# Kernel tuning notes

Hardware: AMD Instinct MI355X
Metric: run time of the kernel (lower is better)

Reference implementation:

```python
import jax, jax.numpy as jnp
import numpy as np

B, SQ, SK = 2, 2048, 2048
D = 1024            # in_features == num_heads * head_size
H, HS = 16, 64      # num_heads, head_size
SCALE = HS ** -0.5


def setup_inputs() -> dict:
    key = jax.random.key(0)
    ks = jax.random.split(key, 10)
    s = 0.02
    return {
        "inputs": jax.random.normal(ks[0], (B, SQ, D), jnp.float32),
        "context": jax.random.normal(ks[1], (B, SK, D), jnp.float32),
        "Wq": jax.random.normal(ks[2], (D, D), jnp.float32) * s,
        "bq": jnp.zeros((D,), jnp.float32),
        "Wk": jax.random.normal(ks[3], (D, D), jnp.float32) * s,
        "bk": jnp.zeros((D,), jnp.float32),
        "Wv": jax.random.normal(ks[4], (D, D), jnp.float32) * s,
        "bv": jnp.zeros((D,), jnp.float32),
        "Wo": jax.random.normal(ks[5], (D, D), jnp.float32) * s,
        "bo": jnp.zeros((D,), jnp.float32),
    }


def reference(inputs, context, Wq, bq, Wk, bk, Wv, bv, Wo, bo):
    # QKV projections (torch Linear: x @ W.T + b; here W stored as [in, out])
    q = inputs @ Wq + bq            # [B, SQ, D]
    k = context @ Wk + bk           # [B, SK, D]
    v = context @ Wv + bv           # [B, SK, D]
    q = q.reshape(B, SQ, H, HS)
    k = k.reshape(B, SK, H, HS)
    v = v.reshape(B, SK, H, HS)
    # scores: [B, H, SQ, SK] -- full score matrix materialized (as in source)
    score = jnp.einsum("bqhd,bkhd->bhqk", q, k) * SCALE
    weights = jax.nn.softmax(score, axis=-1)
    attn = jnp.einsum("bhqk,bkhd->bqhd", weights, v)  # [B, SQ, H, HS]
    out = attn.reshape(B, SQ, H * HS)
    return out @ Wo + bo
```

## Files before the change

kernel.cpp:

```cpp
#include <hip/hip_runtime.h>

#define BB 2
#define SQ 2048
#define SK 2048
#define DD 1024
#define HH 16
#define HS 64
#define SCALE 0.125f
#define LOG2E 1.4426950408889634f

typedef __bf16 bf16x8 __attribute__((ext_vector_type(8)));
typedef float f32x4 __attribute__((ext_vector_type(4)));
typedef unsigned int uint;

#if defined(__has_builtin)
#if __has_builtin(__builtin_amdgcn_exp2f)
#define FEXP2(x) __builtin_amdgcn_exp2f(x)
#endif
#endif
#ifndef FEXP2
extern "C" __device__ float __ocml_native_exp2_f32(float);
#define FEXP2(x) __ocml_native_exp2_f32(x)
#endif

__device__ __forceinline__ void gload_lds16(const __bf16* g, __bf16* l) {
    __builtin_amdgcn_global_load_lds((const __attribute__((address_space(1))) uint*)(g),
                                     (__attribute__((address_space(3))) uint*)(l), 16, 0, 0);
}

__global__ void wtrans(const float* __restrict__ W0, const float* __restrict__ W1,
                       const float* __restrict__ W2, const float* __restrict__ W3,
                       __bf16* __restrict__ Wt) {
    __shared__ __bf16 tile[32][33];
    const float* W = blockIdx.z == 0 ? W0 : blockIdx.z == 1 ? W1 : blockIdx.z == 2 ? W2 : W3;
    __bf16* out = Wt + (size_t)blockIdx.z * DD * DD;
    int tx = threadIdx.x, ty = threadIdx.y;
    int k0 = blockIdx.y * 32, n0 = blockIdx.x * 32;
#pragma unroll
    for (int j = 0; j < 4; ++j)
        tile[ty + j * 8][tx] = (__bf16)W[(size_t)(k0 + ty + j * 8) * DD + n0 + tx];
    __syncthreads();
#pragma unroll
    for (int j = 0; j < 4; ++j) {
        int n = n0 + ty + j * 8;
        int k = k0 + tx;
        int kswz = (k & ~63) | ((((k >> 3) ^ n) & 7) << 3) | (k & 7);
        out[(size_t)n * DD + kswz] = tile[tx][ty + j * 8];
    }
}

__global__ __launch_bounds__(256, 4) void gemm_qkv(
        const float* __restrict__ Ain, const float* __restrict__ Actx,
        const __bf16* __restrict__ Wt,
        const float* __restrict__ bq, const float* __restrict__ bk, const float* __restrict__ bv,
        __bf16* __restrict__ Qb, __bf16* __restrict__ Kb, __bf16* __restrict__ Vtb,
        float qscale) {
    __shared__ __bf16 As[64][64];
    __shared__ __bf16 Bs[128][64];
    int t = threadIdx.x, w = t >> 6, l = t & 63;
    int lm = l & 15, lk = l >> 4;
    int wr = w >> 1, wc = w & 1;
    int flat = blockIdx.x + 16 * blockIdx.y;
    int nf = (flat & 7) * 192 + (flat >> 3);
    bool isQ = nf < 512;
    int bc, br;
    if (isQ) { bc = nf & 7; br = nf >> 3; }
    else     { int f = nf - 512; bc = f & 15; br = f >> 4; }

    int ra = t >> 2, ca = (t & 3) * 2;
    const float* ag = (isQ ? Ain : Actx) + (size_t)(br * 64 + ra) * 1024 + ca * 8;
    __bf16* aw0 = &As[ra][((ca)     ^ (ra & 7)) * 8];
    __bf16* aw1 = &As[ra][((ca + 1) ^ (ra & 7)) * 8];

    int rb = t >> 3, c8 = t & 7;
    const __bf16 *bg0, *bg1, *bg2, *bg3;
    if (isQ) {
        const __bf16* Wq_ = Wt;
        bg0 = Wq_ + (size_t)(bc * 128 + rb)      * 1024 + c8 * 8;
        bg1 = Wq_ + (size_t)(bc * 128 + rb + 32) * 1024 + c8 * 8;
        bg2 = Wq_ + (size_t)(bc * 128 + rb + 64) * 1024 + c8 * 8;
        bg3 = Wq_ + (size_t)(bc * 128 + rb + 96) * 1024 + c8 * 8;
    } else {
        const __bf16* Wk_ = Wt + (size_t)DD * DD;
        const __bf16* Wv_ = Wt + (size_t)2 * DD * DD;
        bg0 = Wk_ + (size_t)(bc * 64 + rb)      * 1024 + c8 * 8;
        bg1 = Wk_ + (size_t)(bc * 64 + rb + 32) * 1024 + c8 * 8;
        bg2 = Wv_ + (size_t)(bc * 64 + rb)      * 1024 + c8 * 8;
        bg3 = Wv_ + (size_t)(bc * 64 + rb + 32) * 1024 + c8 * 8;
    }
    __bf16* bw0 = &Bs[rb][c8 * 8];
    __bf16* bw1 = &Bs[rb + 32][c8 * 8];
    __bf16* bw2 = &Bs[rb + 64][c8 * 8];
    __bf16* bw3 = &Bs[rb + 96][c8 * 8];

    int brow[4];
#pragma unroll
    for (int n = 0; n < 4; ++n)
        brow[n] = isQ ? (wc * 64 + n * 16 + lm)
                      : ((n >> 1) * 64 + wc * 32 + (n & 1) * 16 + lm);

    float4 xa0, xa1, xa2, xa3, xb0, xb1, xb2, xb3;
#define G_LOAD()                                                                      \
    xa0 = *(const float4*)(ag);     xa1 = *(const float4*)(ag + 4);                   \
    xa2 = *(const float4*)(ag + 8); xa3 = *(const float4*)(ag + 12);                  \
    xb0 = *(const float4*)bg0; xb1 = *(const float4*)bg1;                             \
    xb2 = *(const float4*)bg2; xb3 = *(const float4*)bg3;                             \
    ag += 64; bg0 += 64; bg1 += 64; bg2 += 64; bg3 += 64;
#define G_WRITE()                                                                     \
    {                                                                                 \
        bf16x8 va0 = {(__bf16)xa0.x, (__bf16)xa0.y, (__bf16)xa0.z, (__bf16)xa0.w,     \
                      (__bf16)xa1.x, (__bf16)xa1.y, (__bf16)xa1.z, (__bf16)xa1.w};    \
        bf16x8 va1 = {(__bf16)xa2.x, (__bf16)xa2.y, (__bf16)xa2.z, (__bf16)xa2.w,     \
                      (__bf16)xa3.x, (__bf16)xa3.y, (__bf16)xa3.z, (__bf16)xa3.w};    \
        *(bf16x8*)aw0 = va0; *(bf16x8*)aw1 = va1;                                     \
        *(float4*)bw0 = xb0; *(float4*)bw1 = xb1;                                     \
        *(float4*)bw2 = xb2; *(float4*)bw3 = xb3;                                     \
    }

    f32x4 acc[2][4] = {};
    G_LOAD();
    for (int kt = 0; kt < 1024; kt += 64) {
        __syncthreads();
        G_WRITE();
        __syncthreads();
        if (kt + 64 < 1024) { G_LOAD(); }
#pragma unroll
        for (int kk = 0; kk < 64; kk += 32) {
            int ch = ((kk >> 3) + lk);
            bf16x8 af[2], bf[4];
#pragma unroll
            for (int m = 0; m < 2; ++m)
                af[m] = *(const bf16x8*)&As[wr * 32 + m * 16 + lm][(ch ^ (lm & 7)) * 8];
#pragma unroll
            for (int n = 0; n < 4; ++n)
                bf[n] = *(const bf16x8*)&Bs[brow[n]][(ch ^ (lm & 7)) * 8];
#pragma unroll
            for (int m = 0; m < 2; ++m)
#pragma unroll
                for (int n = 0; n < 4; ++n)
                    acc[m][n] = __builtin_amdgcn_mfma_f32_16x16x32_bf16(af[m], bf[n], acc[m][n], 0, 0, 0);
        }
    }
#undef G_LOAD
#undef G_WRITE

    if (isQ) {
#pragma unroll
        for (int m = 0; m < 2; ++m)
#pragma unroll
            for (int n = 0; n < 4; ++n) {
                int col = bc * 128 + wc * 64 + n * 16 + lm;
                float bb = bq[col];
#pragma unroll
                for (int r = 0; r < 4; ++r) {
                    int row = br * 64 + wr * 32 + m * 16 + lk * 4 + r;
                    Qb[(size_t)row * 1024 + col] = (__bf16)((acc[m][n][r] + bb) * qscale);
                }
            }
    } else {
#pragma unroll
        for (int m = 0; m < 2; ++m)
#pragma unroll
            for (int n = 0; n < 4; ++n) {
                int col = bc * 64 + wc * 32 + (n & 1) * 16 + lm;
                if (n < 2) {
                    float bb = bk[col];
#pragma unroll
                    for (int r = 0; r < 4; ++r) {
                        int row = br * 64 + wr * 32 + m * 16 + lk * 4 + r;
                        Kb[(size_t)row * 1024 + col] = (__bf16)(acc[m][n][r] + bb);
                    }
                } else {
                    float bb = bv[col];
                    int row = br * 64 + wr * 32 + m * 16 + lk * 4;
                    int b_ = row >> 11, sk = row & 2047;
                    int skb = sk & ~63, o = sk & 63;
                    int p0 = (o & 32) | (((o >> 3) & 1) << 4) | (((o >> 2) & 1) << 3) | (((o >> 4) & 1) << 2);
                    int h_ = col >> 6, d_ = col & 63;
                    union { ushort4 u; __bf16 hh[4]; } pk;
#pragma unroll
                    for (int r = 0; r < 4; ++r) pk.hh[r] = (__bf16)(acc[m][n][r] + bb);
                    *(ushort4*)(Vtb + ((size_t)((b_ * 16 + h_) * 64 + d_) * 2048 + skb + p0)) = pk.u;
                }
            }
    }
}

__global__ __launch_bounds__(256) void gemm_out64(const __bf16* __restrict__ A, const __bf16* __restrict__ Bt,
                                                  const float* __restrict__ bias, float* __restrict__ C) {
    __shared__ __bf16 As[64][64];
    __shared__ __bf16 Bs[128][64];
    int t = threadIdx.x;
    int w = t >> 6, l = t & 63;
    int lm = l & 15, lk = l >> 4;
    int flat = blockIdx.x + 8 * blockIdx.y;
    int nf = (flat & 7) * 64 + (flat >> 3);
    int bc = nf & 7, br = nf >> 3;
    int srow = (l >> 3), scol = (l & 7) * 8;
    f32x4 acc[4][2] = {};
    for (int kt = 0; kt < 1024; kt += 64) {
        __syncthreads();
#pragma unroll
        for (int j = 0; j < 2; ++j) {
            int r0 = (j * 4 + w) * 8;
            gload_lds16(&A[(size_t)(br * 64 + r0 + srow) * 1024 + kt + scol], &As[r0][0]);
        }
#pragma unroll
        for (int j = 0; j < 4; ++j) {
            int r0 = (j * 4 + w) * 8;
            gload_lds16(&Bt[(size_t)(bc * 128 + r0 + srow) * 1024 + kt + scol], &Bs[r0][0]);
        }
        __syncthreads();
#pragma unroll
        for (int kk = 0; kk < 64; kk += 32) {
            int ch = ((kk >> 3) + lk);
            bf16x8 af[4], bf[2];
#pragma unroll
            for (int m = 0; m < 4; ++m) af[m] = *(const bf16x8*)&As[m * 16 + lm][kk + lk * 8];
#pragma unroll
            for (int n = 0; n < 2; ++n)
                bf[n] = *(const bf16x8*)&Bs[w * 32 + n * 16 + lm][(ch ^ (lm & 7)) * 8];
#pragma unroll
            for (int m = 0; m < 4; ++m)
#pragma unroll
                for (int n = 0; n < 2; ++n)
                    acc[m][n] = __builtin_amdgcn_mfma_f32_16x16x32_bf16(af[m], bf[n], acc[m][n], 0, 0, 0);
        }
    }
#pragma unroll
    for (int m = 0; m < 4; ++m)
#pragma unroll
        for (int n = 0; n < 2; ++n) {
            int col = bc * 128 + w * 32 + n * 16 + lm;
            float bv = bias[col];
#pragma unroll
            for (int r = 0; r < 4; ++r) {
                int row = br * 64 + m * 16 + lk * 4 + r;
                C[(size_t)row * 1024 + col] = acc[m][n][r] + bv;
            }
        }
}

__global__ __launch_bounds__(512) void flash_attn(const __bf16* __restrict__ Q,
                                                  const __bf16* __restrict__ Kb,
                                                  const __bf16* __restrict__ Vt,
                                                  __bf16* __restrict__ O) {
    __shared__ __bf16 Ks[2][64 * 64];
    __shared__ __bf16 Vs[2][64 * 64];
    int t = threadIdx.x, w = t >> 6, l = t & 63;
    int lm = l & 15, lk = l >> 4;
    int flat = blockIdx.x + 16 * blockIdx.y;
    int nf = (flat & 7) * 64 + (flat >> 3);
    int bh = nf >> 4, b = bh >> 4, h = bh & 15;
    int q0 = (nf & 15) * 128;

    bf16x8 qf[2];
#pragma unroll
    for (int kk = 0; kk < 2; ++kk)
        qf[kk] = *(const bf16x8*)&Q[(size_t)(b * SQ + q0 + w * 16 + lm) * DD + h * HS + kk * 32 + lk * 8];

    int r0 = t >> 3, c8 = t & 7;
    int chs = c8 ^ (r0 & 7);
    __bf16* ksl0 = &Ks[0][r0 * 64 + chs * 8];
    __bf16* vsl0 = &Vs[0][r0 * 64 + chs * 8];

    const __bf16* kp0 = Kb + (size_t)b * SK * DD + h * HS + (size_t)r0 * DD + c8 * 8;
    const __bf16* vp0 = Vt + (size_t)bh * HS * SK + (size_t)r0 * SK + c8 * 8;

    int o0 = lm * 64 + ((lk ^ (lm & 7)) * 8);
    int o1 = lm * 64 + (((4 + lk) ^ (lm & 7)) * 8);

    float4 kr0, vr0;
#define FA_LOAD()                                                                \
    kr0 = *(const float4*)kp0; vr0 = *(const float4*)vp0;                        \
    kp0 += (size_t)64 * DD; vp0 += 64;
#define FA_WRITE(BUF)                                                            \
    *(float4*)(ksl0 + (BUF) * 4096) = kr0;                                       \
    *(float4*)(vsl0 + (BUF) * 4096) = vr0;

    FA_LOAD();
    FA_WRITE(0);
    __syncthreads();

    bf16x8 ones;
#pragma unroll
    for (int j = 0; j < 8; ++j) ones[j] = (__bf16)1.0f;

    f32x4 o[4] = {};
    f32x4 o_s = {};

    for (int it = 0; it < 32; ++it) {
        int buf = it & 1;
        if (it + 1 < 32) { FA_LOAD(); }

        const __bf16* KsB = &Ks[buf][0];
        const __bf16* VsB = &Vs[buf][0];

        f32x4 st[4] = {};
        __builtin_amdgcn_s_setprio(1);
#pragma unroll
        for (int kk = 0; kk < 2; ++kk) {
#pragma unroll
            for (int n = 0; n < 4; ++n) {
                bf16x8 kf = *(const bf16x8*)&KsB[(kk ? o1 : o0) + n * 1024];
                st[n] = __builtin_amdgcn_mfma_f32_16x16x32_bf16(kf, qf[kk], st[n], 0, 0, 0);
            }
        }
        __builtin_amdgcn_s_setprio(0);

#pragma unroll
        for (int kk = 0; kk < 2; ++kk) {
            bf16x8 pa;
#pragma unroll
            for (int j = 0; j < 8; ++j)
                pa[j] = (__bf16)FEXP2(st[2 * kk + (j >> 2)][j & 3]);
            __builtin_amdgcn_s_setprio(1);
            o_s = __builtin_amdgcn_mfma_f32_16x16x32_bf16(pa, ones, o_s, 0, 0, 0);
#pragma unroll
            for (int dn = 0; dn < 4; ++dn) {
                bf16x8 vf = *(const bf16x8*)&VsB[(kk ? o1 : o0) + dn * 1024];
                o[dn] = __builtin_amdgcn_mfma_f32_16x16x32_bf16(pa, vf, o[dn], 0, 0, 0);
            }
            __builtin_amdgcn_s_setprio(0);
        }

        if (it + 1 < 32) { FA_WRITE(buf ^ 1); }
        __syncthreads();
    }

    f32x4 inv;
#pragma unroll
    for (int r = 0; r < 4; ++r) inv[r] = 1.f / o_s[r];
#pragma unroll
    for (int dn = 0; dn < 4; ++dn)
#pragma unroll
        for (int r = 0; r < 4; ++r) {
            int row = q0 + w * 16 + lk * 4 + r;
            int col = h * HS + dn * 16 + lm;
            O[(size_t)(b * SQ + row) * DD + col] = (__bf16)(o[dn][r] * inv[r]);
        }
}

extern "C" void kernel_launch(void* const* d_in, const int* in_sizes, int n_in,
                              void* d_out, int out_size, void* d_ws, size_t ws_size,
                              hipStream_t stream) {
    const float* inputs  = (const float*)d_in[0];
    const float* context = (const float*)d_in[1];
    const float* Wq = (const float*)d_in[2];
    const float* bq = (const float*)d_in[3];
    const float* Wk = (const float*)d_in[4];
    const float* bk = (const float*)d_in[5];
    const float* Wv = (const float*)d_in[6];
    const float* bv = (const float*)d_in[7];
    const float* Wo = (const float*)d_in[8];
    const float* bo = (const float*)d_in[9];
    float* out = (float*)d_out;

    char* ws = (char*)d_ws;
    const size_t SEG = (size_t)4096 * 1024 * sizeof(__bf16);
    __bf16* attb = (__bf16*)(ws + 0 * SEG);
    __bf16* Wt   = (__bf16*)(ws + 2 * SEG);
    __bf16* Qb   = (__bf16*)(ws + 3 * SEG);
    __bf16* Kbuf = (__bf16*)(ws + 4 * SEG);
    __bf16* Vtb  = (__bf16*)(ws + 5 * SEG);

    wtrans<<<dim3(32, 32, 4), dim3(32, 8), 0, stream>>>(Wq, Wk, Wv, Wo, Wt);

    gemm_qkv<<<dim3(16, 96), 256, 0, stream>>>(inputs, context, Wt, bq, bk, bv,
                                               Qb, Kbuf, Vtb, SCALE * LOG2E);

    flash_attn<<<dim3(16, 32), 512, 0, stream>>>(Qb, Kbuf, Vtb, attb);

    gemm_out64<<<dim3(8, 64), 256, 0, stream>>>(attb, Wt + (size_t)3 * DD * DD, bo, out);
}
```

Before: 113.8 us.

## Double-buffer shared memory in QKV projection GEMM to drop one barrier

Double-buffers the A and B shared-memory tiles in the QKV projection GEMM. The next tile's global loads are issued before the MFMA loop and written into the alternate buffer afterward, so each iteration needs one barrier instead of two. This doubles LDS use (48KB per block) and lowers the launch-bounds occupancy hint from 4 to 3 blocks, which may cut latency hiding.

```diff
diff --git a/kernel.cpp b/kernel.cpp
--- a/kernel.cpp
+++ b/kernel.cpp
@@ -49,14 +49,14 @@
     }
 }
 
-__global__ __launch_bounds__(256, 4) void gemm_qkv(
+__global__ __launch_bounds__(256, 3) void gemm_qkv(
         const float* __restrict__ Ain, const float* __restrict__ Actx,
         const __bf16* __restrict__ Wt,
         const float* __restrict__ bq, const float* __restrict__ bk, const float* __restrict__ bv,
         __bf16* __restrict__ Qb, __bf16* __restrict__ Kb, __bf16* __restrict__ Vtb,
         float qscale) {
-    __shared__ __bf16 As[64][64];
-    __shared__ __bf16 Bs[128][64];
+    __shared__ __bf16 As[2 * 64 * 64];
+    __shared__ __bf16 Bs[2 * 128 * 64];
     int t = threadIdx.x, w = t >> 6, l = t & 63;
     int lm = l & 15, lk = l >> 4;
     int wr = w >> 1, wc = w & 1;
@@ -69,8 +69,8 @@
 
     int ra = t >> 2, ca = (t & 3) * 2;
     const float* ag = (isQ ? Ain : Actx) + (size_t)(br * 64 + ra) * 1024 + ca * 8;
-    __bf16* aw0 = &As[ra][((ca)     ^ (ra & 7)) * 8];
-    __bf16* aw1 = &As[ra][((ca + 1) ^ (ra & 7)) * 8];
+    __bf16* aw0 = &As[ra * 64 + ((ca)     ^ (ra & 7)) * 8];
+    __bf16* aw1 = &As[ra * 64 + ((ca + 1) ^ (ra & 7)) * 8];
 
     int rb = t >> 3, c8 = t & 7;
     const __bf16 *bg0, *bg1, *bg2, *bg3;
@@ -88,10 +88,10 @@
         bg2 = Wv_ + (size_t)(bc * 64 + rb)      * 1024 + c8 * 8;
         bg3 = Wv_ + (size_t)(bc * 64 + rb + 32) * 1024 + c8 * 8;
     }
-    __bf16* bw0 = &Bs[rb][c8 * 8];
-    __bf16* bw1 = &Bs[rb + 32][c8 * 8];
-    __bf16* bw2 = &Bs[rb + 64][c8 * 8];
-    __bf16* bw3 = &Bs[rb + 96][c8 * 8];
+    __bf16* bw0 = &Bs[(rb)      * 64 + c8 * 8];
+    __bf16* bw1 = &Bs[(rb + 32) * 64 + c8 * 8];
+    __bf16* bw2 = &Bs[(rb + 64) * 64 + c8 * 8];
+    __bf16* bw3 = &Bs[(rb + 96) * 64 + c8 * 8];
 
     int brow[4];
 #pragma unroll
@@ -106,40 +106,46 @@
     xb0 = *(const float4*)bg0; xb1 = *(const float4*)bg1;                             \
     xb2 = *(const float4*)bg2; xb3 = *(const float4*)bg3;                             \
     ag += 64; bg0 += 64; bg1 += 64; bg2 += 64; bg3 += 64;
-#define G_WRITE()                                                                     \
+#define G_WRITE(BUF)                                                                  \
     {                                                                                 \
         bf16x8 va0 = {(__bf16)xa0.x, (__bf16)xa0.y, (__bf16)xa0.z, (__bf16)xa0.w,     \
                       (__bf16)xa1.x, (__bf16)xa1.y, (__bf16)xa1.z, (__bf16)xa1.w};    \
         bf16x8 va1 = {(__bf16)xa2.x, (__bf16)xa2.y, (__bf16)xa2.z, (__bf16)xa2.w,     \
                       (__bf16)xa3.x, (__bf16)xa3.y, (__bf16)xa3.z, (__bf16)xa3.w};    \
-        *(bf16x8*)aw0 = va0; *(bf16x8*)aw1 = va1;                                     \
-        *(float4*)bw0 = xb0; *(float4*)bw1 = xb1;                                     \
-        *(float4*)bw2 = xb2; *(float4*)bw3 = xb3;                                     \
+        *(bf16x8*)(aw0 + (BUF) * 4096) = va0;                                         \
+        *(bf16x8*)(aw1 + (BUF) * 4096) = va1;                                         \
+        *(float4*)(bw0 + (BUF) * 8192) = xb0;                                         \
+        *(float4*)(bw1 + (BUF) * 8192) = xb1;                                         \
+        *(float4*)(bw2 + (BUF) * 8192) = xb2;                                         \
+        *(float4*)(bw3 + (BUF) * 8192) = xb3;                                         \
     }
 
     f32x4 acc[2][4] = {};
     G_LOAD();
+    G_WRITE(0);
+    __syncthreads();
     for (int kt = 0; kt < 1024; kt += 64) {
-        __syncthreads();
-        G_WRITE();
-        __syncthreads();
-        if (kt + 64 < 1024) { G_LOAD(); }
+        int buf = (kt >> 6) & 1;
+        bool more = (kt + 64 < 1024);
+        if (more) { G_LOAD(); }
 #pragma unroll
         for (int kk = 0; kk < 64; kk += 32) {
             int ch = ((kk >> 3) + lk);
             bf16x8 af[2], bf[4];
 #pragma unroll
             for (int m = 0; m < 2; ++m)
-                af[m] = *(const bf16x8*)&As[wr * 32 + m * 16 + lm][(ch ^ (lm & 7)) * 8];
+                af[m] = *(const bf16x8*)&As[buf * 4096 + (wr * 32 + m * 16 + lm) * 64 + (ch ^ (lm & 7)) * 8];
 #pragma unroll
             for (int n = 0; n < 4; ++n)
-                bf[n] = *(const bf16x8*)&Bs[brow[n]][(ch ^ (lm & 7)) * 8];
+                bf[n] = *(const bf16x8*)&Bs[buf * 8192 + brow[n] * 64 + (ch ^ (lm & 7)) * 8];
 #pragma unroll
             for (int m = 0; m < 2; ++m)
 #pragma unroll
                 for (int n = 0; n < 4; ++n)
                     acc[m][n] = __builtin_amdgcn_mfma_f32_16x16x32_bf16(af[m], bf[n], acc[m][n], 0, 0, 0);
         }
+        if (more) { G_WRITE(buf ^ 1); }
+        __syncthreads();
     }
 #undef G_LOAD
 #undef G_WRITE
```

Measured after the change: 117.4 us. 1.03x slower.

## Double-buffer QKV and output GEMMs with direct global-to-LDS loads

Applied to the files above, without the earlier changes.

Both projection GEMMs now use two LDS buffers, issuing global_load_lds for the next K tile while MFMAs run on the current one, with one barrier per iteration instead of two. The QKV GEMM stages raw fp32 activations into LDS with an XOR swizzle and converts to bf16 at fragment-read time, dropping the register round trip. The output GEMM gains an A-side swizzle that the bf16 tile previously lacked. The cost is twice the LDS per block (the QKV A buffer grows further because it holds fp32), which can reduce occupancy; the QKV kernel also drops its min-blocks launch bound.

```diff
diff --git a/kernel.cpp b/kernel.cpp
--- a/kernel.cpp
+++ b/kernel.cpp
@@ -27,6 +27,10 @@
     __builtin_amdgcn_global_load_lds((const __attribute__((address_space(1))) uint*)(g),
                                      (__attribute__((address_space(3))) uint*)(l), 16, 0, 0);
 }
+__device__ __forceinline__ void gload_lds16f(const float* g, float* l) {
+    __builtin_amdgcn_global_load_lds((const __attribute__((address_space(1))) uint*)(g),
+                                     (__attribute__((address_space(3))) uint*)(l), 16, 0, 0);
+}
 
 __global__ void wtrans(const float* __restrict__ W0, const float* __restrict__ W1,
                        const float* __restrict__ W2, const float* __restrict__ W3,
@@ -49,14 +53,14 @@
     }
 }
 
-__global__ __launch_bounds__(256, 4) void gemm_qkv(
+__global__ __launch_bounds__(256) void gemm_qkv(
         const float* __restrict__ Ain, const float* __restrict__ Actx,
         const __bf16* __restrict__ Wt,
         const float* __restrict__ bq, const float* __restrict__ bk, const float* __restrict__ bv,
         __bf16* __restrict__ Qb, __bf16* __restrict__ Kb, __bf16* __restrict__ Vtb,
         float qscale) {
-    __shared__ __bf16 As[64][64];
-    __shared__ __bf16 Bs[128][64];
+    __shared__ float  Asf[2 * 64 * 64];
+    __shared__ __bf16 Bs[2 * 128 * 64];
     int t = threadIdx.x, w = t >> 6, l = t & 63;
     int lm = l & 15, lk = l >> 4;
     int wr = w >> 1, wc = w & 1;
@@ -67,31 +71,29 @@
     if (isQ) { bc = nf & 7; br = nf >> 3; }
     else     { int f = nf - 512; bc = f & 15; br = f >> 4; }
 
-    int ra = t >> 2, ca = (t & 3) * 2;
-    const float* ag = (isQ ? Ain : Actx) + (size_t)(br * 64 + ra) * 1024 + ca * 8;
-    __bf16* aw0 = &As[ra][((ca)     ^ (ra & 7)) * 8];
-    __bf16* aw1 = &As[ra][((ca + 1) ^ (ra & 7)) * 8];
-
-    int rb = t >> 3, c8 = t & 7;
-    const __bf16 *bg0, *bg1, *bg2, *bg3;
+    int rA = t >> 4, cA = t & 15;
+    int csA = cA ^ (2 * (rA & 7));
+    const float* Afp = isQ ? Ain : Actx;
+    const float* agb = Afp + (size_t)(br * 64 + rA) * 1024 + csA * 4;
+    float* adst = &Asf[rA * 64 + cA * 4];
+
+    int rB = t >> 3, cB = t & 7;
+    const __bf16 *bs0, *bs1, *bs2, *bs3;
     if (isQ) {
         const __bf16* Wq_ = Wt;
-        bg0 = Wq_ + (size_t)(bc * 128 + rb)      * 1024 + c8 * 8;
-        bg1 = Wq_ + (size_t)(bc * 128 + rb + 32) * 1024 + c8 * 8;
-        bg2 = Wq_ + (size_t)(bc * 128 + rb + 64) * 1024 + c8 * 8;
-        bg3 = Wq_ + (size_t)(bc * 128 + rb + 96) * 1024 + c8 * 8;
+        bs0 = Wq_ + (size_t)(bc * 128 + rB)      * 1024 + cB * 8;
+        bs1 = Wq_ + (size_t)(bc * 128 + rB + 32) * 1024 + cB * 8;
+        bs2 = Wq_ + (size_t)(bc * 128 + rB + 64) * 1024 + cB * 8;
+        bs3 = Wq_ + (size_t)(bc * 128 + rB + 96) * 1024 + cB * 8;
     } else {
         const __bf16* Wk_ = Wt + (size_t)DD * DD;
         const __bf16* Wv_ = Wt + (size_t)2 * DD * DD;
-        bg0 = Wk_ + (size_t)(bc * 64 + rb)      * 1024 + c8 * 8;
-        bg1 = Wk_ + (size_t)(bc * 64 + rb + 32) * 1024 + c8 * 8;
-        bg2 = Wv_ + (size_t)(bc * 64 + rb)      * 1024 + c8 * 8;
-        bg3 = Wv_ + (size_t)(bc * 64 + rb + 32) * 1024 + c8 * 8;
-    }
-    __bf16* bw0 = &Bs[rb][c8 * 8];
-    __bf16* bw1 = &Bs[rb + 32][c8 * 8];
-    __bf16* bw2 = &Bs[rb + 64][c8 * 8];
-    __bf16* bw3 = &Bs[rb + 96][c8 * 8];
+        bs0 = Wk_ + (size_t)(bc * 64 + rB)      * 1024 + cB * 8;
+        bs1 = Wk_ + (size_t)(bc * 64 + rB + 32) * 1024 + cB * 8;
+        bs2 = Wv_ + (size_t)(bc * 64 + rB)      * 1024 + cB * 8;
+        bs3 = Wv_ + (size_t)(bc * 64 + rB + 32) * 1024 + cB * 8;
+    }
+    __bf16* bdst = &Bs[rB * 64 + cB * 8];
 
     int brow[4];
 #pragma unroll
@@ -99,50 +101,48 @@
         brow[n] = isQ ? (wc * 64 + n * 16 + lm)
                       : ((n >> 1) * 64 + wc * 32 + (n & 1) * 16 + lm);
 
-    float4 xa0, xa1, xa2, xa3, xb0, xb1, xb2, xb3;
-#define G_LOAD()                                                                      \
-    xa0 = *(const float4*)(ag);     xa1 = *(const float4*)(ag + 4);                   \
-    xa2 = *(const float4*)(ag + 8); xa3 = *(const float4*)(ag + 12);                  \
-    xb0 = *(const float4*)bg0; xb1 = *(const float4*)bg1;                             \
-    xb2 = *(const float4*)bg2; xb3 = *(const float4*)bg3;                             \
-    ag += 64; bg0 += 64; bg1 += 64; bg2 += 64; bg3 += 64;
-#define G_WRITE()                                                                     \
-    {                                                                                 \
-        bf16x8 va0 = {(__bf16)xa0.x, (__bf16)xa0.y, (__bf16)xa0.z, (__bf16)xa0.w,     \
-                      (__bf16)xa1.x, (__bf16)xa1.y, (__bf16)xa1.z, (__bf16)xa1.w};    \
-        bf16x8 va1 = {(__bf16)xa2.x, (__bf16)xa2.y, (__bf16)xa2.z, (__bf16)xa2.w,     \
-                      (__bf16)xa3.x, (__bf16)xa3.y, (__bf16)xa3.z, (__bf16)xa3.w};    \
-        *(bf16x8*)aw0 = va0; *(bf16x8*)aw1 = va1;                                     \
-        *(float4*)bw0 = xb0; *(float4*)bw1 = xb1;                                     \
-        *(float4*)bw2 = xb2; *(float4*)bw3 = xb3;                                     \
-    }
+#define STAGE(BUF, KT)                                                                \
+    gload_lds16f(agb + (KT),             adst + (BUF) * 4096);                        \
+    gload_lds16f(agb + 16384 + (KT),     adst + (BUF) * 4096 + 1024);                 \
+    gload_lds16f(agb + 32768 + (KT),     adst + (BUF) * 4096 + 2048);                 \
+    gload_lds16f(agb + 49152 + (KT),     adst + (BUF) * 4096 + 3072);                 \
+    gload_lds16(bs0 + (KT), bdst + (BUF) * 8192);                                     \
+    gload_lds16(bs1 + (KT), bdst + (BUF) * 8192 + 2048);                              \
+    gload_lds16(bs2 + (KT), bdst + (BUF) * 8192 + 4096);                              \
+    gload_lds16(bs3 + (KT), bdst + (BUF) * 8192 + 6144);
 
     f32x4 acc[2][4] = {};
-    G_LOAD();
-    for (int kt = 0; kt < 1024; kt += 64) {
-        __syncthreads();
-        G_WRITE();
-        __syncthreads();
-        if (kt + 64 < 1024) { G_LOAD(); }
-#pragma unroll
-        for (int kk = 0; kk < 64; kk += 32) {
-            int ch = ((kk >> 3) + lk);
+    STAGE(0, 0);
+    __syncthreads();
+    for (int ts = 0; ts < 16; ++ts) {
+        int buf = ts & 1;
+        if (ts + 1 < 16) { STAGE(buf ^ 1, (ts + 1) * 64); }
+#pragma unroll
+        for (int kk = 0; kk < 2; ++kk) {
             bf16x8 af[2], bf[4];
 #pragma unroll
-            for (int m = 0; m < 2; ++m)
-                af[m] = *(const bf16x8*)&As[wr * 32 + m * 16 + lm][(ch ^ (lm & 7)) * 8];
+            for (int m = 0; m < 2; ++m) {
+                int rr = wr * 32 + m * 16 + lm;
+                int c0 = (kk * 8 + 2 * lk) ^ (2 * (lm & 7));
+                const float* ap = &Asf[buf * 4096 + rr * 64 + c0 * 4];
+                f32x4 lo = *(const f32x4*)ap;
+                f32x4 hi = *(const f32x4*)(ap + 4);
+                af[m] = bf16x8{(__bf16)lo[0], (__bf16)lo[1], (__bf16)lo[2], (__bf16)lo[3],
+                               (__bf16)hi[0], (__bf16)hi[1], (__bf16)hi[2], (__bf16)hi[3]};
+            }
+            int ch = kk * 4 + lk;
 #pragma unroll
             for (int n = 0; n < 4; ++n)
-                bf[n] = *(const bf16x8*)&Bs[brow[n]][(ch ^ (lm & 7)) * 8];
+                bf[n] = *(const bf16x8*)&Bs[buf * 8192 + brow[n] * 64 + ((ch ^ (lm & 7)) * 8)];
 #pragma unroll
             for (int m = 0; m < 2; ++m)
 #pragma unroll
                 for (int n = 0; n < 4; ++n)
                     acc[m][n] = __builtin_amdgcn_mfma_f32_16x16x32_bf16(af[m], bf[n], acc[m][n], 0, 0, 0);
         }
-    }
-#undef G_LOAD
-#undef G_WRITE
+        __syncthreads();
+    }
+#undef STAGE
 
     if (isQ) {
 #pragma unroll
@@ -188,45 +188,55 @@
 
 __global__ __launch_bounds__(256) void gemm_out64(const __bf16* __restrict__ A, const __bf16* __restrict__ Bt,
                                                   const float* __restrict__ bias, float* __restrict__ C) {
-    __shared__ __bf16 As[64][64];
-    __shared__ __bf16 Bs[128][64];
+    __shared__ __bf16 As[2 * 64 * 64];
+    __shared__ __bf16 Bs[2 * 128 * 64];
     int t = threadIdx.x;
     int w = t >> 6, l = t & 63;
     int lm = l & 15, lk = l >> 4;
     int flat = blockIdx.x + 8 * blockIdx.y;
     int nf = (flat & 7) * 64 + (flat >> 3);
     int bc = nf & 7, br = nf >> 3;
-    int srow = (l >> 3), scol = (l & 7) * 8;
+
+    int rA = t >> 3, cA = t & 7;
+    int csA = cA ^ (rA & 7);
+    const __bf16* as0 = A + (size_t)(br * 64 + rA) * 1024 + csA * 8;
+    __bf16* adst = &As[rA * 64 + cA * 8];
+    const __bf16* bs0 = Bt + (size_t)(bc * 128 + rA) * 1024 + cA * 8;
+    __bf16* bdst = &Bs[rA * 64 + cA * 8];
+
+#define STAGE(BUF, KT)                                                                \
+    gload_lds16(as0 + (KT),             adst + (BUF) * 4096);                         \
+    gload_lds16(as0 + 32768 + (KT),     adst + (BUF) * 4096 + 2048);                  \
+    gload_lds16(bs0 + (KT),             bdst + (BUF) * 8192);                         \
+    gload_lds16(bs0 + 32768 + (KT),     bdst + (BUF) * 8192 + 2048);                  \
+    gload_lds16(bs0 + 65536 + (KT),     bdst + (BUF) * 8192 + 4096);                  \
+    gload_lds16(bs0 + 98304 + (KT),     bdst + (BUF) * 8192 + 6144);
+
     f32x4 acc[4][2] = {};
-    for (int kt = 0; kt < 1024; kt += 64) {
-        __syncthreads();
-#pragma unroll
-        for (int j = 0; j < 2; ++j) {
-            int r0 = (j * 4 + w) * 8;
-            gload_lds16(&A[(size_t)(br * 64 + r0 + srow) * 1024 + kt + scol], &As[r0][0]);
-        }
-#pragma unroll
-        for (int j = 0; j < 4; ++j) {
-            int r0 = (j * 4 + w) * 8;
-            gload_lds16(&Bt[(size_t)(bc * 128 + r0 + srow) * 1024 + kt + scol], &Bs[r0][0]);
-        }
-        __syncthreads();
-#pragma unroll
-        for (int kk = 0; kk < 64; kk += 32) {
-            int ch = ((kk >> 3) + lk);
+    STAGE(0, 0);
+    __syncthreads();
+    for (int ts = 0; ts < 16; ++ts) {
+        int buf = ts & 1;
+        if (ts + 1 < 16) { STAGE(buf ^ 1, (ts + 1) * 64); }
+#pragma unroll
+        for (int kk = 0; kk < 2; ++kk) {
+            int ch = kk * 4 + lk;
             bf16x8 af[4], bf[2];
 #pragma unroll
-            for (int m = 0; m < 4; ++m) af[m] = *(const bf16x8*)&As[m * 16 + lm][kk + lk * 8];
+            for (int m = 0; m < 4; ++m)
+                af[m] = *(const bf16x8*)&As[buf * 4096 + (m * 16 + lm) * 64 + ((ch ^ (lm & 7)) * 8)];
 #pragma unroll
             for (int n = 0; n < 2; ++n)
-                bf[n] = *(const bf16x8*)&Bs[w * 32 + n * 16 + lm][(ch ^ (lm & 7)) * 8];
+                bf[n] = *(const bf16x8*)&Bs[buf * 8192 + (w * 32 + n * 16 + lm) * 64 + ((ch ^ (lm & 7)) * 8)];
 #pragma unroll
             for (int m = 0; m < 4; ++m)
 #pragma unroll
                 for (int n = 0; n < 2; ++n)
                     acc[m][n] = __builtin_amdgcn_mfma_f32_16x16x32_bf16(af[m], bf[n], acc[m][n], 0, 0, 0);
         }
-    }
+        __syncthreads();
+    }
+#undef STAGE
 #pragma unroll
     for (int m = 0; m < 4; ++m)
 #pragma unroll
```

Result: slower. 124.3 us (+9.2%).

## Enlarge QKV projection GEMM tile to 128 rows per block

Applied to the files above, without the earlier changes.

The QKV projection GEMM now computes 128-row tiles per block instead of 64, so each wave holds a 4x4 grid of MFMA accumulators and the grid is halved to 768 blocks. This reuses each loaded weight tile across twice as many activation rows, cutting global weight traffic and LDS B-fragment loads per MFMA. In exchange, register and LDS use per block grow (launch bounds drop to 3 blocks per SM), and fewer blocks may reduce latency hiding and wave balance across the CUs.

```diff
diff --git a/kernel.cpp b/kernel.cpp
--- a/kernel.cpp
+++ b/kernel.cpp
@@ -49,49 +49,45 @@
     }
 }
 
-__global__ __launch_bounds__(256, 4) void gemm_qkv(
+__global__ __launch_bounds__(256, 3) void gemm_qkv(
         const float* __restrict__ Ain, const float* __restrict__ Actx,
         const __bf16* __restrict__ Wt,
         const float* __restrict__ bq, const float* __restrict__ bk, const float* __restrict__ bv,
         __bf16* __restrict__ Qb, __bf16* __restrict__ Kb, __bf16* __restrict__ Vtb,
         float qscale) {
-    __shared__ __bf16 As[64][64];
-    __shared__ __bf16 Bs[128][64];
+    __shared__ __bf16 As[128 * 64];
+    __shared__ __bf16 Bs[128 * 64];
     int t = threadIdx.x, w = t >> 6, l = t & 63;
     int lm = l & 15, lk = l >> 4;
     int wr = w >> 1, wc = w & 1;
     int flat = blockIdx.x + 16 * blockIdx.y;
-    int nf = (flat & 7) * 192 + (flat >> 3);
-    bool isQ = nf < 512;
+    int nf = (flat & 7) * 96 + (flat >> 3);
+    bool isQ = nf < 256;
     int bc, br;
     if (isQ) { bc = nf & 7; br = nf >> 3; }
-    else     { int f = nf - 512; bc = f & 15; br = f >> 4; }
-
-    int ra = t >> 2, ca = (t & 3) * 2;
-    const float* ag = (isQ ? Ain : Actx) + (size_t)(br * 64 + ra) * 1024 + ca * 8;
-    __bf16* aw0 = &As[ra][((ca)     ^ (ra & 7)) * 8];
-    __bf16* aw1 = &As[ra][((ca + 1) ^ (ra & 7)) * 8];
-
-    int rb = t >> 3, c8 = t & 7;
+    else     { int f = nf - 256; bc = f & 15; br = f >> 4; }
+
+    int rA = t >> 3, cA = t & 7;
+    const float* Afp = isQ ? Ain : Actx;
+    const float* agb = Afp + (size_t)(br * 128 + rA) * 1024 + cA * 8;
+    __bf16* aw = &As[rA * 64 + ((cA ^ (rA & 7)) * 8)];
+
     const __bf16 *bg0, *bg1, *bg2, *bg3;
     if (isQ) {
         const __bf16* Wq_ = Wt;
-        bg0 = Wq_ + (size_t)(bc * 128 + rb)      * 1024 + c8 * 8;
-        bg1 = Wq_ + (size_t)(bc * 128 + rb + 32) * 1024 + c8 * 8;
-        bg2 = Wq_ + (size_t)(bc * 128 + rb + 64) * 1024 + c8 * 8;
-        bg3 = Wq_ + (size_t)(bc * 128 + rb + 96) * 1024 + c8 * 8;
+        bg0 = Wq_ + (size_t)(bc * 128 + rA)      * 1024 + cA * 8;
+        bg1 = Wq_ + (size_t)(bc * 128 + rA + 32) * 1024 + cA * 8;
+        bg2 = Wq_ + (size_t)(bc * 128 + rA + 64) * 1024 + cA * 8;
+        bg3 = Wq_ + (size_t)(bc * 128 + rA + 96) * 1024 + cA * 8;
     } else {
         const __bf16* Wk_ = Wt + (size_t)DD * DD;
         const __bf16* Wv_ = Wt + (size_t)2 * DD * DD;
-        bg0 = Wk_ + (size_t)(bc * 64 + rb)      * 1024 + c8 * 8;
-        bg1 = Wk_ + (size_t)(bc * 64 + rb + 32) * 1024 + c8 * 8;
-        bg2 = Wv_ + (size_t)(bc * 64 + rb)      * 1024 + c8 * 8;
-        bg3 = Wv_ + (size_t)(bc * 64 + rb + 32) * 1024 + c8 * 8;
-    }
-    __bf16* bw0 = &Bs[rb][c8 * 8];
-    __bf16* bw1 = &Bs[rb + 32][c8 * 8];
-    __bf16* bw2 = &Bs[rb + 64][c8 * 8];
-    __bf16* bw3 = &Bs[rb + 96][c8 * 8];
+        bg0 = Wk_ + (size_t)(bc * 64 + rA)      * 1024 + cA * 8;
+        bg1 = Wk_ + (size_t)(bc * 64 + rA + 32) * 1024 + cA * 8;
+        bg2 = Wv_ + (size_t)(bc * 64 + rA)      * 1024 + cA * 8;
+        bg3 = Wv_ + (size_t)(bc * 64 + rA + 32) * 1024 + cA * 8;
+    }
+    __bf16* bw = &Bs[rA * 64 + cA * 8];
 
     int brow[4];
 #pragma unroll
@@ -99,43 +95,48 @@
         brow[n] = isQ ? (wc * 64 + n * 16 + lm)
                       : ((n >> 1) * 64 + wc * 32 + (n & 1) * 16 + lm);
 
-    float4 xa0, xa1, xa2, xa3, xb0, xb1, xb2, xb3;
+    float4 a0l, a0h, a1l, a1h, a2l, a2h, a3l, a3h, xb0, xb1, xb2, xb3;
 #define G_LOAD()                                                                      \
-    xa0 = *(const float4*)(ag);     xa1 = *(const float4*)(ag + 4);                   \
-    xa2 = *(const float4*)(ag + 8); xa3 = *(const float4*)(ag + 12);                  \
+    a0l = *(const float4*)(agb);              a0h = *(const float4*)(agb + 4);        \
+    a1l = *(const float4*)(agb + 32768);      a1h = *(const float4*)(agb + 32772);    \
+    a2l = *(const float4*)(agb + 65536);      a2h = *(const float4*)(agb + 65540);    \
+    a3l = *(const float4*)(agb + 98304);      a3h = *(const float4*)(agb + 98308);    \
     xb0 = *(const float4*)bg0; xb1 = *(const float4*)bg1;                             \
     xb2 = *(const float4*)bg2; xb3 = *(const float4*)bg3;                             \
-    ag += 64; bg0 += 64; bg1 += 64; bg2 += 64; bg3 += 64;
+    agb += 64; bg0 += 64; bg1 += 64; bg2 += 64; bg3 += 64;
+#define CVT8(LO, HI) bf16x8{(__bf16)LO.x, (__bf16)LO.y, (__bf16)LO.z, (__bf16)LO.w,   \
+                            (__bf16)HI.x, (__bf16)HI.y, (__bf16)HI.z, (__bf16)HI.w}
 #define G_WRITE()                                                                     \
     {                                                                                 \
-        bf16x8 va0 = {(__bf16)xa0.x, (__bf16)xa0.y, (__bf16)xa0.z, (__bf16)xa0.w,     \
-                      (__bf16)xa1.x, (__bf16)xa1.y, (__bf16)xa1.z, (__bf16)xa1.w};    \
-        bf16x8 va1 = {(__bf16)xa2.x, (__bf16)xa2.y, (__bf16)xa2.z, (__bf16)xa2.w,     \
-                      (__bf16)xa3.x, (__bf16)xa3.y, (__bf16)xa3.z, (__bf16)xa3.w};    \
-        *(bf16x8*)aw0 = va0; *(bf16x8*)aw1 = va1;                                     \
-        *(float4*)bw0 = xb0; *(float4*)bw1 = xb1;                                     \
-        *(float4*)bw2 = xb2; *(float4*)bw3 = xb3;                                     \
-    }
-
-    f32x4 acc[2][4] = {};
+        *(bf16x8*)(aw)        = CVT8(a0l, a0h);                                       \
+        *(bf16x8*)(aw + 2048) = CVT8(a1l, a1h);                                       \
+        *(bf16x8*)(aw + 4096) = CVT8(a2l, a2h);                                       \
+        *(bf16x8*)(aw + 6144) = CVT8(a3l, a3h);                                       \
+        *(float4*)(bw)        = xb0;                                                  \
+        *(float4*)(bw + 2048) = xb1;                                                  \
+        *(float4*)(bw + 4096) = xb2;                                                  \
+        *(float4*)(bw + 6144) = xb3;                                                  \
+    }
+
+    f32x4 acc[4][4] = {};
     G_LOAD();
-    for (int kt = 0; kt < 1024; kt += 64) {
+    for (int ts = 0; ts < 16; ++ts) {
         __syncthreads();
         G_WRITE();
         __syncthreads();
-        if (kt + 64 < 1024) { G_LOAD(); }
-#pragma unroll
-        for (int kk = 0; kk < 64; kk += 32) {
-            int ch = ((kk >> 3) + lk);
-            bf16x8 af[2], bf[4];
-#pragma unroll
-            for (int m = 0; m < 2; ++m)
-                af[m] = *(const bf16x8*)&As[wr * 32 + m * 16 + lm][(ch ^ (lm & 7)) * 8];
+        if (ts + 1 < 16) { G_LOAD(); }
+#pragma unroll
+        for (int kk = 0; kk < 2; ++kk) {
+            int ch = kk * 4 + lk;
+            bf16x8 af[4], bf[4];
+#pragma unroll
+            for (int m = 0; m < 4; ++m)
+                af[m] = *(const bf16x8*)&As[(wr * 64 + m * 16 + lm) * 64 + ((ch ^ (lm & 7)) * 8)];
 #pragma unroll
             for (int n = 0; n < 4; ++n)
-                bf[n] = *(const bf16x8*)&Bs[brow[n]][(ch ^ (lm & 7)) * 8];
-#pragma unroll
-            for (int m = 0; m < 2; ++m)
+                bf[n] = *(const bf16x8*)&Bs[brow[n] * 64 + ((ch ^ (lm & 7)) * 8)];
+#pragma unroll
+            for (int m = 0; m < 4; ++m)
 #pragma unroll
                 for (int n = 0; n < 4; ++n)
                     acc[m][n] = __builtin_amdgcn_mfma_f32_16x16x32_bf16(af[m], bf[n], acc[m][n], 0, 0, 0);
@@ -143,23 +144,24 @@
     }
 #undef G_LOAD
 #undef G_WRITE
+#undef CVT8
 
     if (isQ) {
 #pragma unroll
-        for (int m = 0; m < 2; ++m)
+        for (int m = 0; m < 4; ++m)
 #pragma unroll
             for (int n = 0; n < 4; ++n) {
                 int col = bc * 128 + wc * 64 + n * 16 + lm;
                 float bb = bq[col];
 #pragma unroll
                 for (int r = 0; r < 4; ++r) {
-                    int row = br * 64 + wr * 32 + m * 16 + lk * 4 + r;
+                    int row = br * 128 + wr * 64 + m * 16 + lk * 4 + r;
                     Qb[(size_t)row * 1024 + col] = (__bf16)((acc[m][n][r] + bb) * qscale);
                 }
             }
     } else {
 #pragma unroll
-        for (int m = 0; m < 2; ++m)
+        for (int m = 0; m < 4; ++m)
 #pragma unroll
             for (int n = 0; n < 4; ++n) {
                 int col = bc * 64 + wc * 32 + (n & 1) * 16 + lm;
@@ -167,12 +169,12 @@
                     float bb = bk[col];
 #pragma unroll
                     for (int r = 0; r < 4; ++r) {
-                        int row = br * 64 + wr * 32 + m * 16 + lk * 4 + r;
+                        int row = br * 128 + wr * 64 + m * 16 + lk * 4 + r;
                         Kb[(size_t)row * 1024 + col] = (__bf16)(acc[m][n][r] + bb);
                     }
                 } else {
                     float bb = bv[col];
-                    int row = br * 64 + wr * 32 + m * 16 + lk * 4;
+                    int row = br * 128 + wr * 64 + m * 16 + lk * 4;
                     int b_ = row >> 11, sk = row & 2047;
                     int skb = sk & ~63, o = sk & 63;
                     int p0 = (o & 32) | (((o >> 3) & 1) << 4) | (((o >> 2) & 1) << 3) | (((o >> 4) & 1) << 2);
@@ -366,7 +368,7 @@
 
     wtrans<<<dim3(32, 32, 4), dim3(32, 8), 0, stream>>>(Wq, Wk, Wv, Wo, Wt);
 
-    gemm_qkv<<<dim3(16, 96), 256, 0, stream>>>(inputs, context, Wt, bq, bk, bv,
+    gemm_qkv<<<dim3(16, 48), 256, 0, stream>>>(inputs, context, Wt, bq, bk, bv,
                                                Qb, Kbuf, Vtb, SCALE * LOG2E);
 
     flash_attn<<<dim3(16, 32), 512, 0, stream>>>(Qb, Kbuf, Vtb, attb);
```

After: 105.2 us (median of 2 runs). 7.6% less time.
